# Optimization experiments

Measured on AMD Instinct MI355X. Metric: run time of the kernel, lower is better.

The kernel has to match this reference:

```python
import jax, jax.numpy as jnp
import numpy as np

B_, T_, D_ = 8, 4096, 1024  # batch, seq_len, input_dim == state_dim


def setup_inputs() -> dict:
    key = jax.random.key(0)
    ks = jax.random.split(key, 9)
    s = 1.0 / np.sqrt(D_)  # nn.Linear default init scale
    return {
        "u":   jax.random.normal(ks[0], (B_, T_, D_), dtype=jnp.float32),
        "WA":  jax.random.uniform(ks[1], (D_, D_), jnp.float32, -s, s),
        "WB":  jax.random.uniform(ks[2], (D_, D_), jnp.float32, -s, s),
        "WAf": jax.random.uniform(ks[3], (D_, D_), jnp.float32, -s, s),
        "WBf": jax.random.uniform(ks[4], (D_, D_), jnp.float32, -s, s),
        "w1":  jax.random.uniform(ks[5], (1, D_), jnp.float32, -s, s),
        "w2":  jax.random.uniform(ks[6], (1, D_), jnp.float32, -s, s),
        "b":   jnp.zeros((1,), dtype=jnp.float32),
        "Wc":  jax.random.uniform(ks[7], (1, D_), jnp.float32, -s, s),
    }


def reference(u, WA, WB, WAf, WBf, w1, w2, b, Wc):
    # NOTE: the torch loop reads x_forward/x_backward from the pre-loop zeros
    # tensor, so A(.)/Af(.) are always applied to zeros. Actual math:
    #   x_f[0] = u[0];      x_f[t]   = B  u[t]    for t >= 1
    #   x_b[T-1] = u[T-1];  x_b[t]   = Bf u[t+1]  for t <= T-2
    bsz, seq_len, _ = u.shape
    xf = jnp.concatenate([u[:, :1], jnp.einsum('btd,ed->bte', u[:, 1:], WB)], axis=1)
    xb = jnp.concatenate([jnp.einsum('btd,ed->bte', u[:, 1:], WBf), u[:, -1:]], axis=1)
    gamma = jax.nn.sigmoid(xf @ w1.T + xb @ w2.T + b)       # (b, t, 1)
    y = gamma * (xf + xb) + (1.0 - gamma) * u               # (b, t, d)
    final_output = jax.nn.sigmoid(y @ Wc.T).reshape(bsz, seq_len)
    return y, gamma, final_output
```

## Files before the change

kernel.cpp:

```cpp
#include <hip/hip_runtime.h>
#include <hip/hip_bf16.h>
#include <cstddef>

#define GLOBAL_AS __attribute__((address_space(1)))
#define LDS_AS __attribute__((address_space(3)))

typedef __bf16 bf16_t;
typedef __bf16 bf16x8 __attribute__((ext_vector_type(8)));
typedef __bf16 bf16x4 __attribute__((ext_vector_type(4)));
typedef float f32x4 __attribute__((ext_vector_type(4)));

static constexpr int Tseq  = 4096;
static constexpr int Dd    = 1024;
static constexpr int Mrows = 8 * 4096;

__global__ __launch_bounds__(256) void k_cast_u(const float* __restrict__ src,
                                                bf16_t* __restrict__ dst) {
    const int i = blockIdx.x * 256 + threadIdx.x;
    float4 v = reinterpret_cast<const float4*>(src)[i];
    bf16x4 o;
    o[0] = (__bf16)v.x; o[1] = (__bf16)v.y; o[2] = (__bf16)v.z; o[3] = (__bf16)v.w;
    reinterpret_cast<bf16x4*>(dst)[i] = o;
}

__global__ __launch_bounds__(256) void k_cast_w(const float* __restrict__ WB,
                                                const float* __restrict__ WBf,
                                                bf16_t* __restrict__ dst) {
    const int i  = blockIdx.x * 256 + threadIdx.x;
    const int e4 = i * 4;
    const float* s = (e4 < 1024 * 1024) ? (WB + e4) : (WBf + (e4 - 1024 * 1024));
    float4 v = *reinterpret_cast<const float4*>(s);
    bf16x4 o;
    o[0] = (__bf16)v.x; o[1] = (__bf16)v.y; o[2] = (__bf16)v.z; o[3] = (__bf16)v.w;
    reinterpret_cast<bf16x4*>(dst)[i] = o;
}

__global__ __launch_bounds__(512, 2) void k_gemm(const bf16_t* __restrict__ A,
                                                 const bf16_t* __restrict__ Bt,
                                                 bf16_t* __restrict__ xf,
                                                 bf16_t* __restrict__ xb) {
    __shared__ __align__(16) char sm[131072];

    const int tid  = threadIdx.x;
    const int wid  = tid >> 6;
    const int lane = tid & 63;
    const int lane15 = lane & 15;
    const int g16  = (lane >> 4) * 16;
    const int wmq  = wid >> 1;
    const int wnq  = wid & 1;

    const int bid0 = blockIdx.x;
    const int swzb = (bid0 & 7) * 128 + (bid0 >> 3);
    const int bcol = swzb & 7;
    const int brow = swzb >> 3;

    const int srow = tid >> 3;
    const int scol = ((tid & 7) ^ (srow & 7)) * 8;
    const bf16_t* gA = A  + ((size_t)brow * 256 + srow) * 1024 + scol;
    const bf16_t* gB = Bt + ((size_t)bcol * 256 + srow) * 1024 + scol;

    char* const smw = sm + wid * 1024;

    f32x4 acc[2][2][2][4] = {};
    bf16x8 afr[2][2], bfr[4][2];

#define STAGE(bufb, isA, h, kt1) do {                                          \
    const bf16_t* _s = ((isA) ? gA : gB) + (size_t)(h) * 131072 + (kt1) * 64;  \
    char* _l = smw + (bufb) * 65536 + ((isA) ? 0 : 32768) + (h) * 16384;       \
    __builtin_amdgcn_global_load_lds((const GLOBAL_AS void*)_s,                \
                                     (LDS_AS void*)_l, 16, 0, 0);              \
    __builtin_amdgcn_global_load_lds((const GLOBAL_AS void*)(_s + 65536),      \
                                     (LDS_AS void*)(_l + 8192), 16, 0, 0);     \
} while (0)

#define RD_A(bufb, mhh) do {                                                   \
    _Pragma("unroll") for (int mi = 0; mi < 2; ++mi) {                         \
      const int rr = wmq * 32 + mi * 16 + lane15;                              \
      const char* _p = sm + (bufb) * 65536 + (mhh) * 16384 + rr * 128;         \
      const int sz = (rr & 7) << 4;                                            \
      _Pragma("unroll") for (int kk = 0; kk < 2; ++kk)                         \
        afr[mi][kk] = *reinterpret_cast<const bf16x8*>(_p + ((kk * 64 + g16) ^ sz)); \
    } } while (0)

#define RD_B(bufb, nhh) do {                                                   \
    _Pragma("unroll") for (int ni = 0; ni < 4; ++ni) {                         \
      const int rr = wnq * 64 + ni * 16 + lane15;                              \
      const char* _p = sm + (bufb) * 65536 + 32768 + (nhh) * 16384 + rr * 128; \
      const int sz = (rr & 7) << 4;                                            \
      _Pragma("unroll") for (int kk = 0; kk < 2; ++kk)                         \
        bfr[ni][kk] = *reinterpret_cast<const bf16x8*>(_p + ((kk * 64 + g16) ^ sz)); \
    } } while (0)

#define MM(MH, NH) do {                                                        \
    __builtin_amdgcn_s_setprio(1);                                             \
    _Pragma("unroll") for (int kk = 0; kk < 2; ++kk)                           \
    _Pragma("unroll") for (int mi = 0; mi < 2; ++mi)                           \
    _Pragma("unroll") for (int ni = 0; ni < 4; ++ni)                           \
      acc[MH][mi][NH][ni] = __builtin_amdgcn_mfma_f32_16x16x32_bf16(           \
          afr[mi][kk], bfr[ni][kk], acc[MH][mi][NH][ni], 0, 0, 0);             \
    __builtin_amdgcn_s_setprio(0);                                             \
} while (0)

#define BARM() asm volatile("s_barrier" ::: "memory")

    STAGE(0, 1, 0, 0);
    STAGE(0, 0, 0, 0);
    STAGE(0, 1, 1, 0);
    STAGE(0, 0, 1, 0);
    asm volatile("s_waitcnt vmcnt(4)" ::: "memory");
    BARM();

#pragma unroll 2
    for (int t = 0; t < 16; ++t) {
        const int buf = t & 1;
        const bool pf = t < 15;
        const int k1 = t + 1;
        RD_A(buf, 0); RD_B(buf, 0);
        if (pf) STAGE(buf ^ 1, 1, 0, k1);
        __builtin_amdgcn_s_barrier();
        MM(0, 0);
        if (pf) { asm volatile("s_waitcnt vmcnt(4)" ::: "memory"); }
        else    { asm volatile("s_waitcnt vmcnt(2)" ::: "memory"); }
        BARM();
        RD_A(buf, 1);
        if (pf) STAGE(buf ^ 1, 0, 0, k1);
        __builtin_amdgcn_s_barrier();
        MM(1, 0);
        if (pf) { asm volatile("s_waitcnt vmcnt(4)" ::: "memory"); }
        else    { asm volatile("s_waitcnt vmcnt(0)" ::: "memory"); }
        BARM();
        RD_B(buf, 1);
        if (pf) STAGE(buf ^ 1, 1, 1, k1);
        __builtin_amdgcn_s_barrier();
        MM(1, 1);
        BARM();
        RD_A(buf, 0);
        if (pf) STAGE(buf ^ 1, 0, 1, k1);
        __builtin_amdgcn_s_barrier();
        MM(0, 1);
        if (pf) { asm volatile("s_waitcnt vmcnt(4)" ::: "memory"); }
        BARM();
    }

    const bool isF  = bcol < 4;
    const int rbase = brow * 256 + wmq * 32 + (lane >> 4) * 4;
    const int cb0   = bcol * 256 + wnq * 64 + lane15;
    #pragma unroll
    for (int mh = 0; mh < 2; ++mh)
    #pragma unroll
    for (int mi = 0; mi < 2; ++mi)
    #pragma unroll
    for (int j = 0; j < 4; ++j) {
        const int r = rbase + mh * 128 + mi * 16 + j;
        #pragma unroll
        for (int nh = 0; nh < 2; ++nh)
        #pragma unroll
        for (int ni = 0; ni < 4; ++ni) {
            const int c = cb0 + nh * 128 + ni * 16;
            const __bf16 v = (__bf16)acc[mh][mi][nh][ni][j];
            if (isF)         xf[(size_t)r * 1024 + c] = v;
            else if (r >= 1) xb[(size_t)(r - 1) * 1024 + (c - 1024)] = v;
        }
    }
#undef STAGE
#undef RD_A
#undef RD_B
#undef MM
#undef BARM
}

__global__ __launch_bounds__(256) void k_epi(const float* __restrict__ u,
                                             const bf16_t* __restrict__ xf,
                                             const bf16_t* __restrict__ xb,
                                             const float* __restrict__ w1,
                                             const float* __restrict__ w2,
                                             const float* __restrict__ bb,
                                             const float* __restrict__ Wc,
                                             float* __restrict__ y,
                                             float* __restrict__ gout,
                                             float* __restrict__ fout) {
    const int lane = threadIdx.x & 63;
    const int row  = blockIdx.x * 4 + (threadIdx.x >> 6);
    const int t    = row & (Tseq - 1);
    const size_t rb = (size_t)row * Dd;

    float uv[16], xfv[16], xbv[16];
    #pragma unroll
    for (int j = 0; j < 2; ++j) {
        const int e = j * 512 + lane * 8;
        const float4 u0 = *reinterpret_cast<const float4*>(u + rb + e);
        const float4 u1 = *reinterpret_cast<const float4*>(u + rb + e + 4);
        uv[j*8+0] = u0.x; uv[j*8+1] = u0.y; uv[j*8+2] = u0.z; uv[j*8+3] = u0.w;
        uv[j*8+4] = u1.x; uv[j*8+5] = u1.y; uv[j*8+6] = u1.z; uv[j*8+7] = u1.w;
        const bf16x8 f8 = *reinterpret_cast<const bf16x8*>(xf + rb + e);
        const bf16x8 b8 = *reinterpret_cast<const bf16x8*>(xb + rb + e);
        #pragma unroll
        for (int i = 0; i < 8; ++i) { xfv[j*8+i] = (float)f8[i]; xbv[j*8+i] = (float)b8[i]; }
    }
    if (t == 0) {
        #pragma unroll
        for (int i = 0; i < 16; ++i) xfv[i] = uv[i];
    }
    if (t == Tseq - 1) {
        #pragma unroll
        for (int i = 0; i < 16; ++i) xbv[i] = uv[i];
    }

    float part = 0.0f;
    #pragma unroll
    for (int j = 0; j < 2; ++j) {
        const int e = j * 512 + lane * 8;
        const float4 a0 = *reinterpret_cast<const float4*>(w1 + e);
        const float4 a1 = *reinterpret_cast<const float4*>(w1 + e + 4);
        const float4 c0 = *reinterpret_cast<const float4*>(w2 + e);
        const float4 c1 = *reinterpret_cast<const float4*>(w2 + e + 4);
        part += xfv[j*8+0]*a0.x + xfv[j*8+1]*a0.y + xfv[j*8+2]*a0.z + xfv[j*8+3]*a0.w
              + xfv[j*8+4]*a1.x + xfv[j*8+5]*a1.y + xfv[j*8+6]*a1.z + xfv[j*8+7]*a1.w
              + xbv[j*8+0]*c0.x + xbv[j*8+1]*c0.y + xbv[j*8+2]*c0.z + xbv[j*8+3]*c0.w
              + xbv[j*8+4]*c1.x + xbv[j*8+5]*c1.y + xbv[j*8+6]*c1.z + xbv[j*8+7]*c1.w;
    }
    #pragma unroll
    for (int off = 32; off >= 1; off >>= 1) part += __shfl_xor(part, off);
    const float g = 1.0f / (1.0f + __expf(-(part + bb[0])));

    float p2 = 0.0f;
    #pragma unroll
    for (int j = 0; j < 2; ++j) {
        const int e = j * 512 + lane * 8;
        float4 y0, y1;
        y0.x = g * (xfv[j*8+0] + xbv[j*8+0]) + (1.0f - g) * uv[j*8+0];
        y0.y = g * (xfv[j*8+1] + xbv[j*8+1]) + (1.0f - g) * uv[j*8+1];
        y0.z = g * (xfv[j*8+2] + xbv[j*8+2]) + (1.0f - g) * uv[j*8+2];
        y0.w = g * (xfv[j*8+3] + xbv[j*8+3]) + (1.0f - g) * uv[j*8+3];
        y1.x = g * (xfv[j*8+4] + xbv[j*8+4]) + (1.0f - g) * uv[j*8+4];
        y1.y = g * (xfv[j*8+5] + xbv[j*8+5]) + (1.0f - g) * uv[j*8+5];
        y1.z = g * (xfv[j*8+6] + xbv[j*8+6]) + (1.0f - g) * uv[j*8+6];
        y1.w = g * (xfv[j*8+7] + xbv[j*8+7]) + (1.0f - g) * uv[j*8+7];
        *reinterpret_cast<float4*>(y + rb + e)     = y0;
        *reinterpret_cast<float4*>(y + rb + e + 4) = y1;
        const float4 wc0 = *reinterpret_cast<const float4*>(Wc + e);
        const float4 wc1 = *reinterpret_cast<const float4*>(Wc + e + 4);
        p2 += y0.x*wc0.x + y0.y*wc0.y + y0.z*wc0.z + y0.w*wc0.w
            + y1.x*wc1.x + y1.y*wc1.y + y1.z*wc1.z + y1.w*wc1.w;
    }
    #pragma unroll
    for (int off = 32; off >= 1; off >>= 1) p2 += __shfl_xor(p2, off);
    if (lane == 0) {
        gout[row] = g;
        fout[row] = 1.0f / (1.0f + __expf(-p2));
    }
}

extern "C" void kernel_launch(void* const* d_in, const int* in_sizes, int n_in,
                              void* d_out, int out_size, void* d_ws, size_t ws_size,
                              hipStream_t stream) {
    const float* u   = (const float*)d_in[0];
    const float* WB  = (const float*)d_in[2];
    const float* WBf = (const float*)d_in[4];
    const float* w1  = (const float*)d_in[5];
    const float* w2  = (const float*)d_in[6];
    const float* bb  = (const float*)d_in[7];
    const float* Wc  = (const float*)d_in[8];

    char* ws = (char*)d_ws;
    bf16_t* u16  = (bf16_t*)(ws);
    bf16_t* wcat = (bf16_t*)(ws + 67108864);
    bf16_t* xfw  = (bf16_t*)(ws + 71303168);
    bf16_t* xbw  = (bf16_t*)(ws + 138412032);

    float* y    = (float*)d_out;
    float* gout = y + (size_t)Mrows * Dd;
    float* fout = gout + Mrows;

    k_cast_u<<<dim3(32768), dim3(256), 0, stream>>>(u, u16);
    k_cast_w<<<dim3(2048),  dim3(256), 0, stream>>>(WB, WBf, wcat);

    k_gemm<<<dim3(1024), dim3(512), 0, stream>>>(u16, wcat, xfw, xbw);

    k_epi<<<dim3(Mrows / 4), dim3(256), 0, stream>>>(u, xfw, xbw, w1, w2, bb, Wc,
                                                     y, gout, fout);
}
```

Measured before the change: 444.9 us.

## Merge cast kernels, keep A fragments, and read bf16 u in epilogue

The two cast kernels become one launch. The GEMM now keeps the A fragments for both M halves in registers, so the last phase of each k-step no longer re-reads A from LDS. The epilogue now reads the bf16 copy of u instead of fp32 u, which halves that read traffic. It also processes two rows per wave with the weights hoisted into registers. The trade-offs are higher register pressure in the GEMM and lower precision for the u term in y, which now uses bf16-rounded u.

```diff
diff --git a/kernel.cpp b/kernel.cpp
--- a/kernel.cpp
+++ b/kernel.cpp
@@ -13,26 +13,28 @@
 static constexpr int Tseq  = 4096;
 static constexpr int Dd    = 1024;
 static constexpr int Mrows = 8 * 4096;
-
-__global__ __launch_bounds__(256) void k_cast_u(const float* __restrict__ src,
-                                                bf16_t* __restrict__ dst) {
+static constexpr int UGRP  = 8388608;
+
+__global__ __launch_bounds__(256) void k_prep(const float* __restrict__ u,
+                                              const float* __restrict__ WB,
+                                              const float* __restrict__ WBf,
+                                              bf16_t* __restrict__ u16,
+                                              bf16_t* __restrict__ wcat) {
     const int i = blockIdx.x * 256 + threadIdx.x;
-    float4 v = reinterpret_cast<const float4*>(src)[i];
-    bf16x4 o;
-    o[0] = (__bf16)v.x; o[1] = (__bf16)v.y; o[2] = (__bf16)v.z; o[3] = (__bf16)v.w;
-    reinterpret_cast<bf16x4*>(dst)[i] = o;
-}
-
-__global__ __launch_bounds__(256) void k_cast_w(const float* __restrict__ WB,
-                                                const float* __restrict__ WBf,
-                                                bf16_t* __restrict__ dst) {
-    const int i  = blockIdx.x * 256 + threadIdx.x;
-    const int e4 = i * 4;
-    const float* s = (e4 < 1024 * 1024) ? (WB + e4) : (WBf + (e4 - 1024 * 1024));
-    float4 v = *reinterpret_cast<const float4*>(s);
-    bf16x4 o;
-    o[0] = (__bf16)v.x; o[1] = (__bf16)v.y; o[2] = (__bf16)v.z; o[3] = (__bf16)v.w;
-    reinterpret_cast<bf16x4*>(dst)[i] = o;
+    if (i < UGRP) {
+        float4 v = reinterpret_cast<const float4*>(u)[i];
+        bf16x4 o;
+        o[0] = (__bf16)v.x; o[1] = (__bf16)v.y; o[2] = (__bf16)v.z; o[3] = (__bf16)v.w;
+        reinterpret_cast<bf16x4*>(u16)[i] = o;
+    } else {
+        const int j  = i - UGRP;
+        const int e4 = j * 4;
+        const float* s = (e4 < 1024 * 1024) ? (WB + e4) : (WBf + (e4 - 1024 * 1024));
+        float4 v = *reinterpret_cast<const float4*>(s);
+        bf16x4 o;
+        o[0] = (__bf16)v.x; o[1] = (__bf16)v.y; o[2] = (__bf16)v.z; o[3] = (__bf16)v.w;
+        reinterpret_cast<bf16x4*>(wcat)[j] = o;
+    }
 }
 
 __global__ __launch_bounds__(512, 2) void k_gemm(const bf16_t* __restrict__ A,
@@ -62,7 +64,8 @@
     char* const smw = sm + wid * 1024;
 
     f32x4 acc[2][2][2][4] = {};
-    bf16x8 afr[2][2], bfr[4][2];
+    bf16x8 afr[2][2][2];
+    bf16x8 bfr[4][2];
 
 #define STAGE(bufb, isA, h, kt1) do {                                          \
     const bf16_t* _s = ((isA) ? gA : gB) + (size_t)(h) * 131072 + (kt1) * 64;  \
@@ -79,7 +82,7 @@
       const char* _p = sm + (bufb) * 65536 + (mhh) * 16384 + rr * 128;         \
       const int sz = (rr & 7) << 4;                                            \
       _Pragma("unroll") for (int kk = 0; kk < 2; ++kk)                         \
-        afr[mi][kk] = *reinterpret_cast<const bf16x8*>(_p + ((kk * 64 + g16) ^ sz)); \
+        afr[mhh][mi][kk] = *reinterpret_cast<const bf16x8*>(_p + ((kk * 64 + g16) ^ sz)); \
     } } while (0)
 
 #define RD_B(bufb, nhh) do {                                                   \
@@ -97,7 +100,7 @@
     _Pragma("unroll") for (int mi = 0; mi < 2; ++mi)                           \
     _Pragma("unroll") for (int ni = 0; ni < 4; ++ni)                           \
       acc[MH][mi][NH][ni] = __builtin_amdgcn_mfma_f32_16x16x32_bf16(           \
-          afr[mi][kk], bfr[ni][kk], acc[MH][mi][NH][ni], 0, 0, 0);             \
+          afr[MH][mi][kk], bfr[ni][kk], acc[MH][mi][NH][ni], 0, 0, 0);         \
     __builtin_amdgcn_s_setprio(0);                                             \
 } while (0)
 
@@ -134,7 +137,6 @@
         __builtin_amdgcn_s_barrier();
         MM(1, 1);
         BARM();
-        RD_A(buf, 0);
         if (pf) STAGE(buf ^ 1, 0, 1, k1);
         __builtin_amdgcn_s_barrier();
         MM(0, 1);
@@ -169,7 +171,7 @@
 #undef BARM
 }
 
-__global__ __launch_bounds__(256) void k_epi(const float* __restrict__ u,
+__global__ __launch_bounds__(256) void k_epi(const bf16_t* __restrict__ u16,
                                              const bf16_t* __restrict__ xf,
                                              const bf16_t* __restrict__ xb,
                                              const float* __restrict__ w1,
@@ -180,74 +182,98 @@
                                              float* __restrict__ gout,
                                              float* __restrict__ fout) {
     const int lane = threadIdx.x & 63;
-    const int row  = blockIdx.x * 4 + (threadIdx.x >> 6);
-    const int t    = row & (Tseq - 1);
-    const size_t rb = (size_t)row * Dd;
-
-    float uv[16], xfv[16], xbv[16];
+    const int r0   = blockIdx.x * 8 + (threadIdx.x >> 6) * 2;
+
+    bf16x8 u8[2][2], f8[2][2], b8[2][2];
+    #pragma unroll
+    for (int rr = 0; rr < 2; ++rr) {
+        const size_t rb = (size_t)(r0 + rr) * Dd;
+        #pragma unroll
+        for (int j = 0; j < 2; ++j) {
+            const int e = j * 512 + lane * 8;
+            u8[rr][j] = *reinterpret_cast<const bf16x8*>(u16 + rb + e);
+            f8[rr][j] = *reinterpret_cast<const bf16x8*>(xf + rb + e);
+            b8[rr][j] = *reinterpret_cast<const bf16x8*>(xb + rb + e);
+        }
+    }
+    float w1v[16], w2v[16], wcv[16];
     #pragma unroll
     for (int j = 0; j < 2; ++j) {
         const int e = j * 512 + lane * 8;
-        const float4 u0 = *reinterpret_cast<const float4*>(u + rb + e);
-        const float4 u1 = *reinterpret_cast<const float4*>(u + rb + e + 4);
-        uv[j*8+0] = u0.x; uv[j*8+1] = u0.y; uv[j*8+2] = u0.z; uv[j*8+3] = u0.w;
-        uv[j*8+4] = u1.x; uv[j*8+5] = u1.y; uv[j*8+6] = u1.z; uv[j*8+7] = u1.w;
-        const bf16x8 f8 = *reinterpret_cast<const bf16x8*>(xf + rb + e);
-        const bf16x8 b8 = *reinterpret_cast<const bf16x8*>(xb + rb + e);
-        #pragma unroll
-        for (int i = 0; i < 8; ++i) { xfv[j*8+i] = (float)f8[i]; xbv[j*8+i] = (float)b8[i]; }
-    }
-    if (t == 0) {
-        #pragma unroll
-        for (int i = 0; i < 16; ++i) xfv[i] = uv[i];
-    }
-    if (t == Tseq - 1) {
-        #pragma unroll
-        for (int i = 0; i < 16; ++i) xbv[i] = uv[i];
-    }
-
-    float part = 0.0f;
-    #pragma unroll
-    for (int j = 0; j < 2; ++j) {
-        const int e = j * 512 + lane * 8;
-        const float4 a0 = *reinterpret_cast<const float4*>(w1 + e);
-        const float4 a1 = *reinterpret_cast<const float4*>(w1 + e + 4);
-        const float4 c0 = *reinterpret_cast<const float4*>(w2 + e);
-        const float4 c1 = *reinterpret_cast<const float4*>(w2 + e + 4);
-        part += xfv[j*8+0]*a0.x + xfv[j*8+1]*a0.y + xfv[j*8+2]*a0.z + xfv[j*8+3]*a0.w
-              + xfv[j*8+4]*a1.x + xfv[j*8+5]*a1.y + xfv[j*8+6]*a1.z + xfv[j*8+7]*a1.w
-              + xbv[j*8+0]*c0.x + xbv[j*8+1]*c0.y + xbv[j*8+2]*c0.z + xbv[j*8+3]*c0.w
-              + xbv[j*8+4]*c1.x + xbv[j*8+5]*c1.y + xbv[j*8+6]*c1.z + xbv[j*8+7]*c1.w;
-    }
-    #pragma unroll
-    for (int off = 32; off >= 1; off >>= 1) part += __shfl_xor(part, off);
-    const float g = 1.0f / (1.0f + __expf(-(part + bb[0])));
-
-    float p2 = 0.0f;
-    #pragma unroll
-    for (int j = 0; j < 2; ++j) {
-        const int e = j * 512 + lane * 8;
-        float4 y0, y1;
-        y0.x = g * (xfv[j*8+0] + xbv[j*8+0]) + (1.0f - g) * uv[j*8+0];
-        y0.y = g * (xfv[j*8+1] + xbv[j*8+1]) + (1.0f - g) * uv[j*8+1];
-        y0.z = g * (xfv[j*8+2] + xbv[j*8+2]) + (1.0f - g) * uv[j*8+2];
-        y0.w = g * (xfv[j*8+3] + xbv[j*8+3]) + (1.0f - g) * uv[j*8+3];
-        y1.x = g * (xfv[j*8+4] + xbv[j*8+4]) + (1.0f - g) * uv[j*8+4];
-        y1.y = g * (xfv[j*8+5] + xbv[j*8+5]) + (1.0f - g) * uv[j*8+5];
-        y1.z = g * (xfv[j*8+6] + xbv[j*8+6]) + (1.0f - g) * uv[j*8+6];
-        y1.w = g * (xfv[j*8+7] + xbv[j*8+7]) + (1.0f - g) * uv[j*8+7];
-        *reinterpret_cast<float4*>(y + rb + e)     = y0;
-        *reinterpret_cast<float4*>(y + rb + e + 4) = y1;
-        const float4 wc0 = *reinterpret_cast<const float4*>(Wc + e);
-        const float4 wc1 = *reinterpret_cast<const float4*>(Wc + e + 4);
-        p2 += y0.x*wc0.x + y0.y*wc0.y + y0.z*wc0.z + y0.w*wc0.w
-            + y1.x*wc1.x + y1.y*wc1.y + y1.z*wc1.z + y1.w*wc1.w;
-    }
-    #pragma unroll
-    for (int off = 32; off >= 1; off >>= 1) p2 += __shfl_xor(p2, off);
+        #pragma unroll
+        for (int i = 0; i < 8; ++i) {
+            w1v[j*8+i] = w1[e + i];
+            w2v[j*8+i] = w2[e + i];
+            wcv[j*8+i] = Wc[e + i];
+        }
+    }
+
+    float uv[2][16], xfv[2][16], xbv[2][16];
+    #pragma unroll
+    for (int rr = 0; rr < 2; ++rr) {
+        const int t = (r0 + rr) & (Tseq - 1);
+        #pragma unroll
+        for (int j = 0; j < 2; ++j) {
+            #pragma unroll
+            for (int i = 0; i < 8; ++i) {
+                uv[rr][j*8+i]  = (float)u8[rr][j][i];
+                xfv[rr][j*8+i] = (float)f8[rr][j][i];
+                xbv[rr][j*8+i] = (float)b8[rr][j][i];
+            }
+        }
+        if (t == 0) {
+            #pragma unroll
+            for (int i = 0; i < 16; ++i) xfv[rr][i] = uv[rr][i];
+        }
+        if (t == Tseq - 1) {
+            #pragma unroll
+            for (int i = 0; i < 16; ++i) xbv[rr][i] = uv[rr][i];
+        }
+    }
+
+    float part[2] = {0.0f, 0.0f};
+    #pragma unroll
+    for (int rr = 0; rr < 2; ++rr)
+        #pragma unroll
+        for (int i = 0; i < 16; ++i)
+            part[rr] += xfv[rr][i] * w1v[i] + xbv[rr][i] * w2v[i];
+    #pragma unroll
+    for (int off = 32; off >= 1; off >>= 1) {
+        part[0] += __shfl_xor(part[0], off);
+        part[1] += __shfl_xor(part[1], off);
+    }
+    const float bias = bb[0];
+    float g[2];
+    g[0] = 1.0f / (1.0f + __expf(-(part[0] + bias)));
+    g[1] = 1.0f / (1.0f + __expf(-(part[1] + bias)));
+
+    float p2[2] = {0.0f, 0.0f};
+    #pragma unroll
+    for (int rr = 0; rr < 2; ++rr) {
+        const size_t rb = (size_t)(r0 + rr) * Dd;
+        #pragma unroll
+        for (int j = 0; j < 4; ++j) {
+            float4 yv;
+            const int e = (j >> 1) * 512 + lane * 8 + (j & 1) * 4;
+            const int q = (j >> 1) * 8 + (j & 1) * 4;
+            yv.x = g[rr] * (xfv[rr][q+0] + xbv[rr][q+0]) + (1.0f - g[rr]) * uv[rr][q+0];
+            yv.y = g[rr] * (xfv[rr][q+1] + xbv[rr][q+1]) + (1.0f - g[rr]) * uv[rr][q+1];
+            yv.z = g[rr] * (xfv[rr][q+2] + xbv[rr][q+2]) + (1.0f - g[rr]) * uv[rr][q+2];
+            yv.w = g[rr] * (xfv[rr][q+3] + xbv[rr][q+3]) + (1.0f - g[rr]) * uv[rr][q+3];
+            *reinterpret_cast<float4*>(y + rb + e) = yv;
+            p2[rr] += yv.x * wcv[q+0] + yv.y * wcv[q+1] + yv.z * wcv[q+2] + yv.w * wcv[q+3];
+        }
+    }
+    #pragma unroll
+    for (int off = 32; off >= 1; off >>= 1) {
+        p2[0] += __shfl_xor(p2[0], off);
+        p2[1] += __shfl_xor(p2[1], off);
+    }
     if (lane == 0) {
-        gout[row] = g;
-        fout[row] = 1.0f / (1.0f + __expf(-p2));
+        gout[r0]     = g[0];
+        gout[r0 + 1] = g[1];
+        fout[r0]     = 1.0f / (1.0f + __expf(-p2[0]));
+        fout[r0 + 1] = 1.0f / (1.0f + __expf(-p2[1]));
     }
 }
 
@@ -272,11 +298,10 @@
     float* gout = y + (size_t)Mrows * Dd;
     float* fout = gout + Mrows;
 
-    k_cast_u<<<dim3(32768), dim3(256), 0, stream>>>(u, u16);
-    k_cast_w<<<dim3(2048),  dim3(256), 0, stream>>>(WB, WBf, wcat);
+    k_prep<<<dim3(34816), dim3(256), 0, stream>>>(u, WB, WBf, u16, wcat);
 
     k_gemm<<<dim3(1024), dim3(512), 0, stream>>>(u16, wcat, xfw, xbw);
 
-    k_epi<<<dim3(Mrows / 4), dim3(256), 0, stream>>>(u, xfw, xbw, w1, w2, bb, Wc,
+    k_epi<<<dim3(Mrows / 8), dim3(256), 0, stream>>>(u16, xfw, xbw, w1, w2, bb, Wc,
                                                      y, gout, fout);
 }
```

Result: faster. 425.2 us (-4.4%).
